# Kernel optimization log

Measured on AMD Instinct MI355X. Metric: run time of the kernel, lower is better.

## Reference

```python
import jax, jax.numpy as jnp
import numpy as np

D_MODEL = 2048
RANK = 64
BATCH = 16384


def setup_inputs() -> dict:
    key = jax.random.key(0)
    ks = jax.random.split(key, 10)
    s = 1.0 / np.sqrt(D_MODEL)
    x = jax.random.normal(ks[0], (BATCH, D_MODEL), dtype=jnp.float32)
    state_re = jax.random.normal(ks[1], (BATCH, RANK), dtype=jnp.float32)
    state_im = jax.random.normal(ks[2], (BATCH, RANK), dtype=jnp.float32)
    W_dt = jax.random.uniform(ks[3], (RANK, D_MODEL), jnp.float32, -s, s)
    b_dt = jax.random.uniform(ks[4], (RANK,), jnp.float32, -s, s)
    W_ph = jax.random.uniform(ks[5], (RANK, D_MODEL), jnp.float32, -s, s)
    b_ph = jax.random.uniform(ks[6], (RANK,), jnp.float32, -s, s)
    W_B = jax.random.uniform(ks[7], (RANK, D_MODEL), jnp.float32, -s, s)
    sC = 1.0 / np.sqrt(RANK)
    W_C = jax.random.uniform(ks[8], (D_MODEL, RANK), jnp.float32, -sC, sC)
    A_real = jnp.log(jnp.arange(1, RANK + 1, dtype=jnp.float32))
    A_imag = jax.random.normal(ks[9], (RANK,), dtype=jnp.float32)
    return {"x": x, "state_re": state_re, "state_im": state_im,
            "W_dt": W_dt, "b_dt": b_dt, "W_ph": W_ph, "b_ph": b_ph,
            "W_B": W_B, "W_C": W_C, "A_real": A_real, "A_imag": A_imag}


def reference(x, state_re, state_im, W_dt, b_dt, W_ph, b_ph, W_B, W_C, A_real, A_imag):
    # four small GEMMs: [B, d_model] x [d_model, rank]
    dt = jax.nn.softplus(x @ W_dt.T + b_dt)                 # [B, rank]
    phase = jnp.tanh(x @ W_ph.T + b_ph) * jnp.pi            # [B, rank]
    decay = jnp.exp(-dt * jnp.exp(A_real))                  # [B, rank]
    angle = dt * A_imag + phase                              # [B, rank]
    B_val = x @ W_B.T                                        # [B, rank]
    cos = jnp.cos(angle)
    sin = jnp.sin(angle)
    # complex rotate-and-decay state update
    new_re = (state_re * cos - state_im * sin) * decay + B_val
    new_im = (state_re * sin + state_im * cos) * decay
    out = new_re @ W_C.T                                     # [B, d_model]
    return out, new_re, new_im
```

## Files before the change

### kernel.cpp

```cpp
#include <hip/hip_runtime.h>
#include <stdint.h>

#define D_MODEL 2048
#define RANK    64
#define BATCH   16384

#define BM      32
#define KSTEP   64
#define LDA     72

typedef unsigned short u16;
typedef __attribute__((ext_vector_type(8))) short  bf16x8;
typedef __attribute__((ext_vector_type(4))) float  f32x4;
typedef __attribute__((ext_vector_type(4))) unsigned short u16x4;

#define WCAT_HI 0
#define WCAT_LO (192*2048)
#define WC_HI   (2*192*2048)
#define WC_LO   (2*192*2048 + 2048*64)

__device__ __forceinline__ u16 f2bf(float f) {
    uint32_t u = __float_as_uint(f);
    u += 0x7fffu + ((u >> 16) & 1u);
    return (u16)(u >> 16);
}
__device__ __forceinline__ float bf2f(u16 h) {
    return __uint_as_float(((uint32_t)h) << 16);
}

#define MFMA(a, b, c) __builtin_amdgcn_mfma_f32_16x16x32_bf16((a), (b), (c), 0, 0, 0)

__global__ __launch_bounds__(256) void prep_split(
    const float* __restrict__ Wdt, const float* __restrict__ Wph,
    const float* __restrict__ WB,  const float* __restrict__ WC,
    u16* __restrict__ ws)
{
    int t = blockIdx.x * 256 + threadIdx.x;
    if (t < 98304) {
        int i = t << 2;
        int n = i >> 11, k = i & 2047;
        const float* src = (n < 64)  ? (Wdt + n * 2048 + k)
                         : (n < 128) ? (Wph + (n - 64) * 2048 + k)
                                     : (WB  + (n - 128) * 2048 + k);
        f32x4 v = *(const f32x4*)src;
        u16x4 hi, lo;
        #pragma unroll
        for (int j = 0; j < 4; ++j) {
            hi[j] = f2bf(v[j]);
            lo[j] = f2bf(v[j] - bf2f(hi[j]));
        }
        *(u16x4*)(ws + WCAT_HI + i) = hi;
        *(u16x4*)(ws + WCAT_LO + i) = lo;
    } else {
        int i = (t - 98304) << 2;
        f32x4 v = *(const f32x4*)(WC + i);
        u16x4 hi, lo;
        #pragma unroll
        for (int j = 0; j < 4; ++j) {
            hi[j] = f2bf(v[j]);
            lo[j] = f2bf(v[j] - bf2f(hi[j]));
        }
        *(u16x4*)(ws + WC_HI + i) = hi;
        *(u16x4*)(ws + WC_LO + i) = lo;
    }
}

__global__ __launch_bounds__(256, 2) void mamba_fused(
    const float* __restrict__ x,
    const float* __restrict__ state_re, const float* __restrict__ state_im,
    const float* __restrict__ b_dt, const float* __restrict__ b_ph,
    const float* __restrict__ A_real, const float* __restrict__ A_imag,
    const u16* __restrict__ ws,
    float* __restrict__ dout)
{
    __shared__ __align__(16) u16 xa_hi[BM * LDA];
    __shared__ __align__(16) u16 xa_lo[BM * LDA];
    __shared__ __align__(16) u16 nr_hi[BM * LDA];
    __shared__ __align__(16) u16 nr_lo[BM * LDA];

    const u16* wcat_hi = ws + WCAT_HI;
    const u16* wcat_lo = ws + WCAT_LO;
    const u16* wc_hi   = ws + WC_HI;
    const u16* wc_lo   = ws + WC_LO;

    const int tid = threadIdx.x;
    const int w   = tid >> 6;
    const int l15 = tid & 15;
    const int lg  = (tid & 63) >> 4;
    const int r0  = blockIdx.x * BM;

    const int r = (w << 4) + l15;
    const float bdt_r  = b_dt[r];
    const float bph_r  = b_ph[r];
    const float expA_r = expf(A_real[r]);
    const float Aim_r  = A_imag[r];

    f32x4 acc[3][2];
    #pragma unroll
    for (int g = 0; g < 3; ++g)
        #pragma unroll
        for (int m = 0; m < 2; ++m)
            acc[g][m] = (f32x4){0.f, 0.f, 0.f, 0.f};

    const int srow0 = tid >> 4;
    const int sc4   = tid & 15;

    for (int it = 0; it < D_MODEL / KSTEP; ++it) {
        const int k0 = it * KSTEP;
        __syncthreads();
        #pragma unroll
        for (int v = 0; v < 2; ++v) {
            const int row = srow0 + v * 16;
            const f32x4 val = *(const f32x4*)(x + (size_t)(r0 + row) * D_MODEL + k0 + (sc4 << 2));
            u16x4 hi, lo;
            #pragma unroll
            for (int j = 0; j < 4; ++j) {
                hi[j] = f2bf(val[j]);
                lo[j] = f2bf(val[j] - bf2f(hi[j]));
            }
            *(u16x4*)(xa_hi + row * LDA + (sc4 << 2)) = hi;
            *(u16x4*)(xa_lo + row * LDA + (sc4 << 2)) = lo;
        }
        __syncthreads();
        #pragma unroll
        for (int kk = 0; kk < 2; ++kk) {
            bf16x8 ah[2], al[2];
            #pragma unroll
            for (int m = 0; m < 2; ++m) {
                const int off = (m * 16 + l15) * LDA + kk * 32 + lg * 8;
                ah[m] = *(const bf16x8*)(xa_hi + off);
                al[m] = *(const bf16x8*)(xa_lo + off);
            }
            const int kg = k0 + kk * 32 + lg * 8;
            #pragma unroll
            for (int g = 0; g < 3; ++g) {
                const int n = ((g << 2) + w) * 16 + l15;
                const bf16x8 bh = *(const bf16x8*)(wcat_hi + n * 2048 + kg);
                const bf16x8 bl = *(const bf16x8*)(wcat_lo + n * 2048 + kg);
                #pragma unroll
                for (int m = 0; m < 2; ++m) {
                    acc[g][m] = MFMA(ah[m], bh, acc[g][m]);
                    acc[g][m] = MFMA(al[m], bh, acc[g][m]);
                    acc[g][m] = MFMA(ah[m], bl, acc[g][m]);
                }
            }
        }
    }

    float* out_main = dout;
    float* out_nre  = dout + (size_t)BATCH * D_MODEL;
    float* out_nim  = out_nre + (size_t)BATCH * RANK;

    #pragma unroll
    for (int m = 0; m < 2; ++m) {
        #pragma unroll
        for (int j = 0; j < 4; ++j) {
            const int row_local = m * 16 + lg * 4 + j;
            const size_t gb = (size_t)(r0 + row_local);
            const float ydt = acc[0][m][j] + bdt_r;
            const float dtv = fmaxf(ydt, 0.f) + log1pf(expf(-fabsf(ydt)));
            const float yph = acc[1][m][j] + bph_r;
            const float ph  = tanhf(yph) * 3.14159274101257324f;
            const float bval = acc[2][m][j];
            const float decay = expf(-dtv * expA_r);
            const float angle = fmaf(dtv, Aim_r, ph);
            float sn, cs;
            sincosf(angle, &sn, &cs);
            const float sre = state_re[gb * RANK + r];
            const float sim = state_im[gb * RANK + r];
            const float nre = (sre * cs - sim * sn) * decay + bval;
            const float nim = (sre * sn + sim * cs) * decay;
            out_nre[gb * RANK + r] = nre;
            out_nim[gb * RANK + r] = nim;
            const u16 h = f2bf(nre);
            nr_hi[row_local * LDA + r] = h;
            nr_lo[row_local * LDA + r] = f2bf(nre - bf2f(h));
        }
    }
    __syncthreads();

    bf16x8 ah2[2][2], al2[2][2];
    #pragma unroll
    for (int m = 0; m < 2; ++m)
        #pragma unroll
        for (int kk = 0; kk < 2; ++kk) {
            const int off = (m * 16 + l15) * LDA + kk * 32 + lg * 8;
            ah2[m][kk] = *(const bf16x8*)(nr_hi + off);
            al2[m][kk] = *(const bf16x8*)(nr_lo + off);
        }

    const int dbase = w << 9;
    for (int nt = 0; nt < 32; ++nt) {
        const int d = dbase + (nt << 4) + l15;
        bf16x8 bh[2], bl[2];
        #pragma unroll
        for (int kk = 0; kk < 2; ++kk) {
            const int off = (d << 6) + kk * 32 + lg * 8;
            bh[kk] = *(const bf16x8*)(wc_hi + off);
            bl[kk] = *(const bf16x8*)(wc_lo + off);
        }
        f32x4 acc2[2];
        #pragma unroll
        for (int m = 0; m < 2; ++m) {
            acc2[m] = (f32x4){0.f, 0.f, 0.f, 0.f};
            #pragma unroll
            for (int kk = 0; kk < 2; ++kk) {
                acc2[m] = MFMA(ah2[m][kk], bh[kk], acc2[m]);
                acc2[m] = MFMA(al2[m][kk], bh[kk], acc2[m]);
                acc2[m] = MFMA(ah2[m][kk], bl[kk], acc2[m]);
            }
        }
        #pragma unroll
        for (int m = 0; m < 2; ++m)
            #pragma unroll
            for (int j = 0; j < 4; ++j) {
                const int row_local = m * 16 + lg * 4 + j;
                out_main[(size_t)(r0 + row_local) * D_MODEL + d] = acc2[m][j];
            }
    }
}

extern "C" void kernel_launch(void* const* d_in, const int* in_sizes, int n_in,
                              void* d_out, int out_size, void* d_ws, size_t ws_size,
                              hipStream_t stream)
{
    const float* x        = (const float*)d_in[0];
    const float* state_re = (const float*)d_in[1];
    const float* state_im = (const float*)d_in[2];
    const float* W_dt     = (const float*)d_in[3];
    const float* b_dt     = (const float*)d_in[4];
    const float* W_ph     = (const float*)d_in[5];
    const float* b_ph     = (const float*)d_in[6];
    const float* W_B      = (const float*)d_in[7];
    const float* W_C      = (const float*)d_in[8];
    const float* A_real   = (const float*)d_in[9];
    const float* A_imag   = (const float*)d_in[10];
    u16*   ws  = (u16*)d_ws;
    float* out = (float*)d_out;

    prep_split<<<512, 256, 0, stream>>>(W_dt, W_ph, W_B, W_C, ws);
    mamba_fused<<<BATCH / BM, 256, 0, stream>>>(x, state_re, state_im, b_dt, b_ph,
                                                A_real, A_imag, ws, out);
}
```

Before: 363.7 us.

## Load x directly into MFMA B operand, drop LDS staging, use 512-thread blocks

Drops the shared-memory staging of x. Each lane now loads its own 8 consecutive floats of x straight from global memory and splits them into hi/lo bf16 registers. The MFMA operands are swapped (weights as A, activations as B), so the accumulator layout gives each lane 4 consecutive rank or d_model columns for one row. That allows vectorized float4 loads and stores for state, biases, new_re/new_im and the output. Blocks grow to 8 waves, split into 2 row groups × 4 column groups, which removes the per-k-step __syncthreads. The trade-off is uncoalesced-ish strided x loads per lane and no reuse of x across waves via LDS, so each of the 4 column-group waves re-reads x.

```diff
diff --git a/kernel.cpp b/kernel.cpp
--- a/kernel.cpp
+++ b/kernel.cpp
@@ -6,7 +6,6 @@
 #define BATCH   16384
 
 #define BM      32
-#define KSTEP   64
 #define LDA     72
 
 typedef unsigned short u16;
@@ -65,7 +64,7 @@
     }
 }
 
-__global__ __launch_bounds__(256, 2) void mamba_fused(
+__global__ __launch_bounds__(512, 4) void mamba_fused(
     const float* __restrict__ x,
     const float* __restrict__ state_re, const float* __restrict__ state_im,
     const float* __restrict__ b_dt, const float* __restrict__ b_ph,
@@ -73,8 +72,6 @@
     const u16* __restrict__ ws,
     float* __restrict__ dout)
 {
-    __shared__ __align__(16) u16 xa_hi[BM * LDA];
-    __shared__ __align__(16) u16 xa_lo[BM * LDA];
     __shared__ __align__(16) u16 nr_hi[BM * LDA];
     __shared__ __align__(16) u16 nr_lo[BM * LDA];
 
@@ -85,65 +82,44 @@
 
     const int tid = threadIdx.x;
     const int w   = tid >> 6;
+    const int wm  = w >> 2;
+    const int wg  = w & 3;
     const int l15 = tid & 15;
     const int lg  = (tid & 63) >> 4;
     const int r0  = blockIdx.x * BM;
 
-    const int r = (w << 4) + l15;
-    const float bdt_r  = b_dt[r];
-    const float bph_r  = b_ph[r];
-    const float expA_r = expf(A_real[r]);
-    const float Aim_r  = A_imag[r];
-
-    f32x4 acc[3][2];
+    const int brow_l = wm * 16 + l15;
+    const int brow   = r0 + brow_l;
+    const size_t xbase = (size_t)brow * D_MODEL;
+    const int kofs = lg * 8;
+
+    f32x4 acc[3];
     #pragma unroll
-    for (int g = 0; g < 3; ++g)
-        #pragma unroll
-        for (int m = 0; m < 2; ++m)
-            acc[g][m] = (f32x4){0.f, 0.f, 0.f, 0.f};
-
-    const int srow0 = tid >> 4;
-    const int sc4   = tid & 15;
-
-    for (int it = 0; it < D_MODEL / KSTEP; ++it) {
-        const int k0 = it * KSTEP;
-        __syncthreads();
-        #pragma unroll
-        for (int v = 0; v < 2; ++v) {
-            const int row = srow0 + v * 16;
-            const f32x4 val = *(const f32x4*)(x + (size_t)(r0 + row) * D_MODEL + k0 + (sc4 << 2));
-            u16x4 hi, lo;
-            #pragma unroll
-            for (int j = 0; j < 4; ++j) {
-                hi[j] = f2bf(val[j]);
-                lo[j] = f2bf(val[j] - bf2f(hi[j]));
-            }
-            *(u16x4*)(xa_hi + row * LDA + (sc4 << 2)) = hi;
-            *(u16x4*)(xa_lo + row * LDA + (sc4 << 2)) = lo;
-        }
-        __syncthreads();
-        #pragma unroll
-        for (int kk = 0; kk < 2; ++kk) {
-            bf16x8 ah[2], al[2];
-            #pragma unroll
-            for (int m = 0; m < 2; ++m) {
-                const int off = (m * 16 + l15) * LDA + kk * 32 + lg * 8;
-                ah[m] = *(const bf16x8*)(xa_hi + off);
-                al[m] = *(const bf16x8*)(xa_lo + off);
-            }
-            const int kg = k0 + kk * 32 + lg * 8;
-            #pragma unroll
-            for (int g = 0; g < 3; ++g) {
-                const int n = ((g << 2) + w) * 16 + l15;
-                const bf16x8 bh = *(const bf16x8*)(wcat_hi + n * 2048 + kg);
-                const bf16x8 bl = *(const bf16x8*)(wcat_lo + n * 2048 + kg);
-                #pragma unroll
-                for (int m = 0; m < 2; ++m) {
-                    acc[g][m] = MFMA(ah[m], bh, acc[g][m]);
-                    acc[g][m] = MFMA(al[m], bh, acc[g][m]);
-                    acc[g][m] = MFMA(ah[m], bl, acc[g][m]);
-                }
-            }
+    for (int g = 0; g < 3; ++g) acc[g] = (f32x4){0.f, 0.f, 0.f, 0.f};
+
+    #pragma unroll 2
+    for (int it = 0; it < D_MODEL / 32; ++it) {
+        const int kg = it * 32 + kofs;
+        const f32x4 xv0 = *(const f32x4*)(x + xbase + kg);
+        const f32x4 xv1 = *(const f32x4*)(x + xbase + kg + 4);
+        bf16x8 xh, xl;
+        #pragma unroll
+        for (int j = 0; j < 4; ++j) {
+            u16 h0 = f2bf(xv0[j]);
+            u16 h1 = f2bf(xv1[j]);
+            xh[j]     = (short)h0;
+            xh[4 + j] = (short)h1;
+            xl[j]     = (short)f2bf(xv0[j] - bf2f(h0));
+            xl[4 + j] = (short)f2bf(xv1[j] - bf2f(h1));
+        }
+        #pragma unroll
+        for (int g = 0; g < 3; ++g) {
+            const int n = ((g << 2) + wg) * 16 + l15;
+            const bf16x8 wh = *(const bf16x8*)(wcat_hi + (size_t)n * 2048 + kg);
+            const bf16x8 wl = *(const bf16x8*)(wcat_lo + (size_t)n * 2048 + kg);
+            acc[g] = MFMA(wh, xh, acc[g]);
+            acc[g] = MFMA(wl, xh, acc[g]);
+            acc[g] = MFMA(wh, xl, acc[g]);
         }
     }
 
@@ -151,72 +127,64 @@
     float* out_nre  = dout + (size_t)BATCH * D_MODEL;
     float* out_nim  = out_nre + (size_t)BATCH * RANK;
 
+    const int rb = wg * 16 + lg * 4;
+    const f32x4 bdt4 = *(const f32x4*)(b_dt  + rb);
+    const f32x4 bph4 = *(const f32x4*)(b_ph  + rb);
+    const f32x4 Are4 = *(const f32x4*)(A_real + rb);
+    const f32x4 Aim4 = *(const f32x4*)(A_imag + rb);
+    const f32x4 sre4 = *(const f32x4*)(state_re + (size_t)brow * RANK + rb);
+    const f32x4 sim4 = *(const f32x4*)(state_im + (size_t)brow * RANK + rb);
+
+    f32x4 nre4, nim4;
+    u16x4 nh4, nl4;
     #pragma unroll
-    for (int m = 0; m < 2; ++m) {
-        #pragma unroll
-        for (int j = 0; j < 4; ++j) {
-            const int row_local = m * 16 + lg * 4 + j;
-            const size_t gb = (size_t)(r0 + row_local);
-            const float ydt = acc[0][m][j] + bdt_r;
-            const float dtv = fmaxf(ydt, 0.f) + log1pf(expf(-fabsf(ydt)));
-            const float yph = acc[1][m][j] + bph_r;
-            const float ph  = tanhf(yph) * 3.14159274101257324f;
-            const float bval = acc[2][m][j];
-            const float decay = expf(-dtv * expA_r);
-            const float angle = fmaf(dtv, Aim_r, ph);
-            float sn, cs;
-            sincosf(angle, &sn, &cs);
-            const float sre = state_re[gb * RANK + r];
-            const float sim = state_im[gb * RANK + r];
-            const float nre = (sre * cs - sim * sn) * decay + bval;
-            const float nim = (sre * sn + sim * cs) * decay;
-            out_nre[gb * RANK + r] = nre;
-            out_nim[gb * RANK + r] = nim;
-            const u16 h = f2bf(nre);
-            nr_hi[row_local * LDA + r] = h;
-            nr_lo[row_local * LDA + r] = f2bf(nre - bf2f(h));
-        }
-    }
+    for (int j = 0; j < 4; ++j) {
+        const float ydt = acc[0][j] + bdt4[j];
+        const float dtv = fmaxf(ydt, 0.f) + log1pf(expf(-fabsf(ydt)));
+        const float ph  = tanhf(acc[1][j] + bph4[j]) * 3.14159274101257324f;
+        const float decay = expf(-dtv * expf(Are4[j]));
+        const float angle = fmaf(dtv, Aim4[j], ph);
+        float sn, cs;
+        sincosf(angle, &sn, &cs);
+        nre4[j] = (sre4[j] * cs - sim4[j] * sn) * decay + acc[2][j];
+        nim4[j] = (sre4[j] * sn + sim4[j] * cs) * decay;
+        const u16 h = f2bf(nre4[j]);
+        nh4[j] = h;
+        nl4[j] = f2bf(nre4[j] - bf2f(h));
+    }
+    *(f32x4*)(out_nre + (size_t)brow * RANK + rb) = nre4;
+    *(f32x4*)(out_nim + (size_t)brow * RANK + rb) = nim4;
+    *(u16x4*)(nr_hi + brow_l * LDA + rb) = nh4;
+    *(u16x4*)(nr_lo + brow_l * LDA + rb) = nl4;
     __syncthreads();
 
-    bf16x8 ah2[2][2], al2[2][2];
+    bf16x8 nh[2], nl[2];
     #pragma unroll
-    for (int m = 0; m < 2; ++m)
+    for (int kk = 0; kk < 2; ++kk) {
+        const int off = brow_l * LDA + kk * 32 + lg * 8;
+        nh[kk] = *(const bf16x8*)(nr_hi + off);
+        nl[kk] = *(const bf16x8*)(nr_lo + off);
+    }
+
+    #pragma unroll 2
+    for (int nt = 0; nt < 32; ++nt) {
+        const int dt0  = (wg << 9) + (nt << 4);
+        const int drow = dt0 + l15;
+        bf16x8 ch[2], cl[2];
         #pragma unroll
         for (int kk = 0; kk < 2; ++kk) {
-            const int off = (m * 16 + l15) * LDA + kk * 32 + lg * 8;
-            ah2[m][kk] = *(const bf16x8*)(nr_hi + off);
-            al2[m][kk] = *(const bf16x8*)(nr_lo + off);
-        }
-
-    const int dbase = w << 9;
-    for (int nt = 0; nt < 32; ++nt) {
-        const int d = dbase + (nt << 4) + l15;
-        bf16x8 bh[2], bl[2];
+            const int off = (drow << 6) + kk * 32 + lg * 8;
+            ch[kk] = *(const bf16x8*)(wc_hi + off);
+            cl[kk] = *(const bf16x8*)(wc_lo + off);
+        }
+        f32x4 o = (f32x4){0.f, 0.f, 0.f, 0.f};
         #pragma unroll
         for (int kk = 0; kk < 2; ++kk) {
-            const int off = (d << 6) + kk * 32 + lg * 8;
-            bh[kk] = *(const bf16x8*)(wc_hi + off);
-            bl[kk] = *(const bf16x8*)(wc_lo + off);
-        }
-        f32x4 acc2[2];
-        #pragma unroll
-        for (int m = 0; m < 2; ++m) {
-            acc2[m] = (f32x4){0.f, 0.f, 0.f, 0.f};
-            #pragma unroll
-            for (int kk = 0; kk < 2; ++kk) {
-                acc2[m] = MFMA(ah2[m][kk], bh[kk], acc2[m]);
-                acc2[m] = MFMA(al2[m][kk], bh[kk], acc2[m]);
-                acc2[m] = MFMA(ah2[m][kk], bl[kk], acc2[m]);
-            }
-        }
-        #pragma unroll
-        for (int m = 0; m < 2; ++m)
-            #pragma unroll
-            for (int j = 0; j < 4; ++j) {
-                const int row_local = m * 16 + lg * 4 + j;
-                out_main[(size_t)(r0 + row_local) * D_MODEL + d] = acc2[m][j];
-            }
+            o = MFMA(ch[kk], nh[kk], o);
+            o = MFMA(cl[kk], nh[kk], o);
+            o = MFMA(ch[kk], nl[kk], o);
+        }
+        *(f32x4*)(out_main + (size_t)brow * D_MODEL + dt0 + lg * 4) = o;
     }
 }
 
@@ -239,6 +207,6 @@
     float* out = (float*)d_out;
 
     prep_split<<<512, 256, 0, stream>>>(W_dt, W_ph, W_B, W_C, ws);
-    mamba_fused<<<BATCH / BM, 256, 0, stream>>>(x, state_re, state_im, b_dt, b_ph,
+    mamba_fused<<<BATCH / BM, 512, 0, stream>>>(x, state_re, state_im, b_dt, b_ph,
                                                 A_real, A_imag, ws, out);
 }
```

Result: slower. 503.2 us (+38.4%).
